# Optimization experiments

Hardware: AMD Instinct MI355X
Metric: run time of the kernel (lower is better)

Reference implementation:

```python
import jax, jax.numpy as jnp
import numpy as np

B, T, S, N, C, H = 2, 16, 256, 32, 3072, 24
D = C // H  # 128 head_dim
EPS = 1e-6


def _layernorm(x):
    # LayerNorm, elementwise_affine=False, eps=1e-6
    mu = jnp.mean(x, axis=-1, keepdims=True)
    var = jnp.mean(jnp.square(x - mu), axis=-1, keepdims=True)
    return (x - mu) * jax.lax.rsqrt(var + EPS)


def _rmsnorm(x, w):
    # RMSNorm with learnable weight, computed in fp32 (matches x.float() path)
    ms = jnp.mean(jnp.square(x), axis=-1, keepdims=True)
    return x * jax.lax.rsqrt(ms + EPS) * w


def setup_inputs() -> dict:
    key = jax.random.key(0)
    ks = jax.random.split(key, 8)
    f = lambda k, sh: jax.random.normal(k, sh, dtype=jnp.float32)
    sc = 1.0 / np.sqrt(C)
    return {
        "x": f(ks[0], (B, T * S, C)),
        "motion_vec": f(ks[1], (B, T, N, C)),
        "motion_mask": jax.random.uniform(ks[2], (B, T * S), dtype=jnp.float32),
        "w_kv": f(ks[3], (2 * C, C)) * sc,
        "b_kv": jnp.zeros((2 * C,), jnp.float32),
        "w_q": f(ks[4], (C, C)) * sc,
        "b_q": jnp.zeros((C,), jnp.float32),
        "w_o": f(ks[5], (C, C)) * sc,
        "b_o": jnp.zeros((C,), jnp.float32),
        "q_norm_w": jnp.ones((D,), jnp.float32),
        "k_norm_w": jnp.ones((D,), jnp.float32),
    }


def reference(x, motion_vec, motion_mask, w_kv, b_kv, w_q, b_q, w_o, b_o,
              q_norm_w, k_norm_w):
    x_motion = _layernorm(motion_vec)            # [B,T,N,C]
    x_feat = _layernorm(x)                       # [B,T*S,C]

    kv = x_motion @ w_kv.T + b_kv                # [B,T,N,2C]
    kv = kv.reshape(B, T, N, 2, H, D)
    k, v = kv[:, :, :, 0], kv[:, :, :, 1]        # [B,T,N,H,D]

    q = (x_feat @ w_q.T + b_q).reshape(B, T, S, H, D)
    q = _rmsnorm(q, q_norm_w)
    k = _rmsnorm(k, k_norm_w)

    # frame-local cross-attention: queries = spatial tokens, keys = motion tokens
    scale = 1.0 / jnp.sqrt(jnp.float32(D))
    scores = jnp.einsum('btshd,btnhd->bthsn', q, k) * scale  # [B,T,H,S,N]
    probs = jax.nn.softmax(scores, axis=-1)
    attn = jnp.einsum('bthsn,btnhd->btshd', probs, v)        # [B,T,S,H,D]
    attn = attn.reshape(B, T * S, C)

    out = attn @ w_o.T + b_o                     # [B,T*S,C]
    return out * motion_mask[:, :, None]
```

## Files before the change

### kernel.cpp

```cpp
#include <hip/hip_runtime.h>
#include <math.h>

typedef unsigned short u16;
typedef unsigned int u32;
typedef short bf16x8 __attribute__((ext_vector_type(8)));
typedef float f32x4 __attribute__((ext_vector_type(4)));
typedef u16 u16x4 __attribute__((ext_vector_type(4)));
typedef u16 u16x8 __attribute__((ext_vector_type(8)));
typedef u32 u32x4 __attribute__((ext_vector_type(4)));

static __device__ __forceinline__ float b2f(u16 u) {
  union { u32 i; float f; } v; v.i = ((u32)u) << 16; return v.f;
}
static __device__ __forceinline__ float blo(u32 u) {
  union { u32 i; float f; } v; v.i = u << 16; return v.f;
}
static __device__ __forceinline__ float bhi(u32 u) {
  union { u32 i; float f; } v; v.i = u & 0xffff0000u; return v.f;
}
static __device__ __forceinline__ u16 f2b(float f) {
  union { float f; u32 i; } v; v.f = f;
  u32 r = v.i + 0x7fffu + ((v.i >> 16) & 1u);
  return (u16)(r >> 16);
}

static __device__ __forceinline__ void g2l16(const void* g, void* l) {
  typedef __attribute__((address_space(1))) const void gvoid;
  typedef __attribute__((address_space(3))) void lvoid;
  __builtin_amdgcn_global_load_lds((gvoid*)g, (lvoid*)l, 16, 0, 0);
}

__global__ __launch_bounds__(256)
void wcvt_kernel(const float* __restrict__ src, u16* __restrict__ dst, int n4)
{
  for (int i = blockIdx.x * 256 + threadIdx.x; i < n4; i += gridDim.x * 256) {
    f32x4 v = *(const f32x4*)(src + (size_t)i * 4);
    u16x4 w; w.x = f2b(v.x); w.y = f2b(v.y); w.z = f2b(v.z); w.w = f2b(v.w);
    *(u16x4*)(dst + (size_t)i * 4) = w;
  }
}

__global__ __launch_bounds__(256)
void ln_kernel(const float* __restrict__ x, const float* __restrict__ mv,
               u16* __restrict__ xf, u16* __restrict__ xm)
{
  const int row = blockIdx.x, tid = threadIdx.x;
  const float* src; u16* dst;
  if (row < 8192) { src = x + (size_t)row * 3072;          dst = xf + (size_t)row * 3072; }
  else            { src = mv + (size_t)(row - 8192) * 3072; dst = xm + (size_t)(row - 8192) * 3072; }

  f32x4 vals[3];
  #pragma unroll
  for (int i = 0; i < 3; ++i) vals[i] = *(const f32x4*)(src + tid * 4 + i * 1024);

  float s1 = 0.f, s2 = 0.f;
  #pragma unroll
  for (int i = 0; i < 3; ++i) {
    f32x4 v = vals[i];
    s1 += v.x + v.y + v.z + v.w;
    s2 += v.x * v.x + v.y * v.y + v.z * v.z + v.w * v.w;
  }
  #pragma unroll
  for (int o = 32; o > 0; o >>= 1) { s1 += __shfl_down(s1, o); s2 += __shfl_down(s2, o); }
  __shared__ float r1[4], r2[4];
  const int wv = tid >> 6, ln = tid & 63;
  if (ln == 0) { r1[wv] = s1; r2[wv] = s2; }
  __syncthreads();
  const float t1 = r1[0] + r1[1] + r1[2] + r1[3];
  const float t2 = r2[0] + r2[1] + r2[2] + r2[3];
  const float mu = t1 * (1.f / 3072.f);
  const float rs = rsqrtf(t2 * (1.f / 3072.f) - mu * mu + 1e-6f);
  #pragma unroll
  for (int i = 0; i < 3; ++i) {
    f32x4 v = vals[i]; u16x4 w;
    w.x = f2b((v.x - mu) * rs); w.y = f2b((v.y - mu) * rs);
    w.z = f2b((v.z - mu) * rs); w.w = f2b((v.w - mu) * rs);
    *(u16x4*)(dst + tid * 4 + i * 1024) = w;
  }
}

template<int EPI, typename TOUT>
__global__ __launch_bounds__(256, 2)
void gemm256(const u16* __restrict__ A, const u16* __restrict__ Wb,
             const float* __restrict__ bias, const float* __restrict__ mask,
             TOUT* __restrict__ C, int M, int N, int K)
{
  __shared__ __align__(16) u16 L[36864];
  const int tid = threadIdx.x, wave = tid >> 6, lane = tid & 63;

  const int nwg = gridDim.x;
  const int bid = (blockIdx.x & 7) * (nwg >> 3) + (blockIdx.x >> 3);
  const int nbx = N >> 7;
  const int brow = (bid / nbx) << 8;
  const int bcol = (bid % nbx) << 7;
  const int wr = wave >> 1, wc = wave & 1;

  const u16* gA = A + (size_t)brow * K;
  const u16* gB = Wb + (size_t)bcol * K;

  const int srow = tid >> 2;
  const int scol = 8 * ((lane & 3) ^ ((lane >> 3) & 3));
  const int rcoff = 8 * ((lane >> 4) ^ ((lane >> 1) & 3));

  f32x4 acc[8][4] = {};

  auto STAGE = [&](int b, int tk) {
    u16* bufA = &L[b * 12288];
    u16* bufB = bufA + 8192;
    const u16* srcA = gA + tk + scol;
    const u16* srcB = gB + tk + scol;
    #pragma unroll
    for (int j = 0; j < 4; ++j)
      g2l16(srcA + (size_t)(j * 64 + srow) * K, bufA + (j * 64 + wave * 16) * 32);
    #pragma unroll
    for (int j = 0; j < 2; ++j)
      g2l16(srcB + (size_t)(j * 64 + srow) * K, bufB + (j * 64 + wave * 16) * 32);
  };

  auto COMPUTE = [&](int b) {
    const u16* bufA = &L[b * 12288];
    const u16* bufB = bufA + 8192;
    bf16x8 af[8], bfv[4];
    #pragma unroll
    for (int m = 0; m < 8; ++m)
      af[m] = *(const bf16x8*)&bufA[(wr * 128 + m * 16 + (lane & 15)) * 32 + rcoff];
    #pragma unroll
    for (int n = 0; n < 4; ++n)
      bfv[n] = *(const bf16x8*)&bufB[(wc * 64 + n * 16 + (lane & 15)) * 32 + rcoff];
    __builtin_amdgcn_s_setprio(1);
    #pragma unroll
    for (int m = 0; m < 8; ++m)
      #pragma unroll
      for (int n = 0; n < 4; ++n)
        acc[m][n] = __builtin_amdgcn_mfma_f32_16x16x32_bf16(af[m], bfv[n], acc[m][n], 0, 0, 0);
    __builtin_amdgcn_s_setprio(0);
  };

  STAGE(0, 0);
  STAGE(1, 32);
  asm volatile("s_waitcnt vmcnt(6)" ::: "memory");
  __builtin_amdgcn_s_barrier();
  __builtin_amdgcn_sched_barrier(0);

  const int NT = K >> 5;
  int cur = 0;
  for (int t = 0; t < NT; ++t) {
    const bool pf = (t + 2) < NT;
    if (pf) {
      int nb = cur + 2; if (nb >= 3) nb -= 3;
      STAGE(nb, (t + 2) << 5);
    }
    COMPUTE(cur);
    if (pf) asm volatile("s_waitcnt vmcnt(6)" ::: "memory");
    else    asm volatile("s_waitcnt vmcnt(0)" ::: "memory");
    __builtin_amdgcn_s_barrier();
    __builtin_amdgcn_sched_barrier(0);
    if (++cur == 3) cur = 0;
  }

  #pragma unroll
  for (int m = 0; m < 8; ++m) {
    const int row = brow + wr * 128 + m * 16 + ((lane >> 4) << 2);
    #pragma unroll
    for (int n = 0; n < 4; ++n) {
      const int col = bcol + wc * 64 + n * 16 + (lane & 15);
      const float bv = bias[col];
      #pragma unroll
      for (int i = 0; i < 4; ++i) {
        float v = acc[m][n][i] + bv;
        if (EPI == 1) v *= mask[row + i];
        if constexpr (__is_same(TOUT, u16))
          C[(size_t)(row + i) * N + col] = f2b(v);
        else
          C[(size_t)(row + i) * N + col] = v;
      }
    }
  }
}

template<int EPI, typename TOUT>
__global__ __launch_bounds__(256)
void gemm_mixed(const u16* __restrict__ A, const float* __restrict__ W,
                const float* __restrict__ bias, const float* __restrict__ mask,
                TOUT* __restrict__ C, int M, int N, int K)
{
  __shared__ __align__(16) u16 lA[4096];
  __shared__ __align__(16) u16 lB[4096];
  const int tid = threadIdx.x, wave = tid >> 6, lane = tid & 63;
  const int nbx = N >> 7;
  const int brow = (blockIdx.x / nbx) << 7;
  const int bcol = (blockIdx.x % nbx) << 7;
  const int wr = wave >> 1, wc = wave & 1;

  f32x4 acc[4][4] = {};
  const u16* gA = A + (size_t)brow * K;
  const float* gB = W + (size_t)bcol * K;
  const int br = tid >> 1, bk0 = (tid & 1) << 4;
  const float* bsrc0 = gB + (size_t)br * K + bk0;
  u16* bdst = &lB[br * 32 + bk0];

  for (int tk = 0; tk < K; tk += 32) {
    #pragma unroll
    for (int j = 0; j < 2; ++j) {
      const int c = j * 256 + wave * 64 + lane;
      const int r = c >> 2, k8 = (c & 3) << 3;
      g2l16(gA + (size_t)r * K + tk + k8, (char*)lA + (size_t)(j * 256 + wave * 64) * 16);
    }
    {
      const float* src = bsrc0 + tk;
      #pragma unroll
      for (int j = 0; j < 4; ++j) {
        f32x4 v = *(const f32x4*)(src + 4 * j);
        u16x4 w; w.x = f2b(v.x); w.y = f2b(v.y); w.z = f2b(v.z); w.w = f2b(v.w);
        *(u16x4*)(bdst + 4 * j) = w;
      }
    }
    __syncthreads();

    bf16x8 af[4], bfr[4];
    #pragma unroll
    for (int m = 0; m < 4; ++m)
      af[m] = *(const bf16x8*)&lA[(wr * 64 + m * 16 + (lane & 15)) * 32 + ((lane >> 4) << 3)];
    #pragma unroll
    for (int n = 0; n < 4; ++n)
      bfr[n] = *(const bf16x8*)&lB[(wc * 64 + n * 16 + (lane & 15)) * 32 + ((lane >> 4) << 3)];
    #pragma unroll
    for (int m = 0; m < 4; ++m)
      #pragma unroll
      for (int n = 0; n < 4; ++n)
        acc[m][n] = __builtin_amdgcn_mfma_f32_16x16x32_bf16(af[m], bfr[n], acc[m][n], 0, 0, 0);
    __syncthreads();
  }

  #pragma unroll
  for (int m = 0; m < 4; ++m) {
    const int row = brow + wr * 64 + m * 16 + ((lane >> 4) << 2);
    #pragma unroll
    for (int n = 0; n < 4; ++n) {
      const int col = bcol + wc * 64 + n * 16 + (lane & 15);
      const float bv = bias[col];
      #pragma unroll
      for (int i = 0; i < 4; ++i) {
        float v = acc[m][n][i] + bv;
        if (EPI == 1) v *= mask[row + i];
        if constexpr (__is_same(TOUT, u16))
          C[(size_t)(row + i) * N + col] = f2b(v);
        else
          C[(size_t)(row + i) * N + col] = v;
      }
    }
  }
}

__global__ __launch_bounds__(256)
void attn_kernel(const u16* __restrict__ qb, const u16* __restrict__ kvb,
                 const float* __restrict__ qw, const float* __restrict__ kw,
                 u16* __restrict__ attnb)
{
  __shared__ __align__(16) float Ks[32][128];
  __shared__ __align__(16) u32 Vsu[32][64];
  __shared__ float scL[256 * 33];
  const int tid = threadIdx.x;
  const int h = blockIdx.x % 24;
  const int bt = blockIdx.x / 24;

  {
    const int n = tid >> 3, sub = tid & 7;
    const size_t base = (size_t)(bt * 32 + n) * 6144 + (size_t)h * 128;
    const u16* kp = kvb + base + sub * 16;
    const u16* vp = kvb + base + 3072 + sub * 16;
    float kv_[16]; float ss = 0.f;
    u16x8 k0 = *(const u16x8*)kp;
    u16x8 k1 = *(const u16x8*)(kp + 8);
    #pragma unroll
    for (int j = 0; j < 8; ++j) { kv_[j] = b2f(k0[j]); kv_[8 + j] = b2f(k1[j]); }
    #pragma unroll
    for (int j = 0; j < 16; ++j) ss += kv_[j] * kv_[j];
    ss += __shfl_xor(ss, 1); ss += __shfl_xor(ss, 2); ss += __shfl_xor(ss, 4);
    const float krs = rsqrtf(ss * (1.f / 128.f) + 1e-6f);
    #pragma unroll
    for (int j = 0; j < 16; ++j) {
      const int d = sub * 16 + j;
      Ks[n][d] = kv_[j] * krs * kw[d] * qw[d];
    }
    u32x4 v0 = *(const u32x4*)vp;
    u32x4 v1 = *(const u32x4*)(vp + 8);
    #pragma unroll
    for (int j = 0; j < 4; ++j) { Vsu[n][sub * 8 + j] = v0[j]; Vsu[n][sub * 8 + 4 + j] = v1[j]; }
  }
  __syncthreads();

  const u16* qp = qb + (size_t)(bt * 256 + tid) * 3072 + (size_t)h * 128;
  u32 qr[64]; float qss = 0.f;
  #pragma unroll
  for (int i = 0; i < 16; ++i) {
    u32x4 t = ((const u32x4*)qp)[i];
    qr[4 * i + 0] = t.x; qr[4 * i + 1] = t.y; qr[4 * i + 2] = t.z; qr[4 * i + 3] = t.w;
  }
  #pragma unroll
  for (int i = 0; i < 64; ++i) { const float a = blo(qr[i]), b = bhi(qr[i]); qss += a * a + b * b; }
  const float qsc = rsqrtf(qss * (1.f / 128.f) + 1e-6f) * 0.08838834764831845f;

  float* mysc = &scL[tid * 33];
  for (int n2 = 0; n2 < 32; ++n2) {
    const f32x4* kr = (const f32x4*)&Ks[n2][0];
    float dot = 0.f;
    #pragma unroll
    for (int dd = 0; dd < 32; ++dd) {
      const f32x4 kk = kr[dd];
      const u32 a0 = qr[2 * dd], a1 = qr[2 * dd + 1];
      dot += blo(a0) * kk.x + bhi(a0) * kk.y + blo(a1) * kk.z + bhi(a1) * kk.w;
    }
    mysc[n2] = dot * qsc;
  }

  float p[32];
  #pragma unroll
  for (int j = 0; j < 32; ++j) p[j] = mysc[j];
  float mx = p[0];
  #pragma unroll
  for (int j = 1; j < 32; ++j) mx = fmaxf(mx, p[j]);
  float se = 0.f;
  #pragma unroll
  for (int j = 0; j < 32; ++j) { p[j] = expf(p[j] - mx); se += p[j]; }
  const float inv = 1.f / se;
  #pragma unroll
  for (int j = 0; j < 32; ++j) mysc[j] = p[j] * inv;

  u16* op = attnb + (size_t)(bt * 256 + tid) * 3072 + (size_t)h * 128;
  for (int db = 0; db < 16; ++db) {
    float o[8] = {0.f, 0.f, 0.f, 0.f, 0.f, 0.f, 0.f, 0.f};
    for (int n2 = 0; n2 < 32; ++n2) {
      const u32x4 vv = *(const u32x4*)&Vsu[n2][db * 4];
      const float pp = mysc[n2];
      o[0] += pp * blo(vv.x); o[1] += pp * bhi(vv.x);
      o[2] += pp * blo(vv.y); o[3] += pp * bhi(vv.y);
      o[4] += pp * blo(vv.z); o[5] += pp * bhi(vv.z);
      o[6] += pp * blo(vv.w); o[7] += pp * bhi(vv.w);
    }
    u16x8 w;
    #pragma unroll
    for (int j = 0; j < 8; ++j) w[j] = f2b(o[j]);
    *(u16x8*)(op + db * 8) = w;
  }
}

extern "C" void kernel_launch(void* const* d_in, const int* in_sizes, int n_in,
                              void* d_out, int out_size, void* d_ws, size_t ws_size,
                              hipStream_t stream) {
  const float* x    = (const float*)d_in[0];
  const float* mv   = (const float*)d_in[1];
  const float* mask = (const float*)d_in[2];
  const float* wkv  = (const float*)d_in[3];
  const float* bkv  = (const float*)d_in[4];
  const float* wq   = (const float*)d_in[5];
  const float* bq   = (const float*)d_in[6];
  const float* wo   = (const float*)d_in[7];
  const float* bo   = (const float*)d_in[8];
  const float* qnw  = (const float*)d_in[9];
  const float* knw  = (const float*)d_in[10];
  float* out = (float*)d_out;

  char* ws = (char*)d_ws;
  u16* xf   = (u16*)(ws);
  u16* xm   = (u16*)(ws + 50331648);
  u16* qbuf = (u16*)(ws + 56623104);
  u16* kvb  = (u16*)(ws + 106954752);
  u16* wslab = (u16*)(ws + 119537664);

  ln_kernel<<<9216, 256, 0, stream>>>(x, mv, xf, xm);

  if (ws_size >= 157286400u) {
    wcvt_kernel<<<2048, 256, 0, stream>>>(wq, wslab, 3072 * 3072 / 4);
    gemm256<0, u16><<<768, 256, 0, stream>>>(xf, wslab, bq, nullptr, qbuf, 8192, 3072, 3072);
    wcvt_kernel<<<2048, 256, 0, stream>>>(wkv, wslab, 6144 * 3072 / 4);
    gemm256<0, u16><<<192, 256, 0, stream>>>(xm, wslab, bkv, nullptr, kvb, 1024, 6144, 3072);
    attn_kernel<<<768, 256, 0, stream>>>(qbuf, kvb, qnw, knw, xf);
    wcvt_kernel<<<2048, 256, 0, stream>>>(wo, wslab, 3072 * 3072 / 4);
    gemm256<1, float><<<768, 256, 0, stream>>>(xf, wslab, bo, mask, out, 8192, 3072, 3072);
  } else {
    gemm_mixed<0, u16><<<1536, 256, 0, stream>>>(xf, wq, bq, nullptr, qbuf, 8192, 3072, 3072);
    gemm_mixed<0, u16><<<384, 256, 0, stream>>>(xm, wkv, bkv, nullptr, kvb, 1024, 6144, 3072);
    attn_kernel<<<768, 256, 0, stream>>>(qbuf, kvb, qnw, knw, xf);
    gemm_mixed<1, float><<<1536, 256, 0, stream>>>(xf, wo, bo, mask, out, 8192, 3072, 3072);
  }
}
```

Baseline: 567.4 us.

## Rewrite frame-local attention with bf16 MFMA for QK and PV

Replaces the scalar per-thread attention kernel with an MFMA-based version. Normalized K and transposed V are staged in LDS as bf16. Each wave handles 64 query rows in 16-row tiles, computing scores and P·V with 16x16x32 bf16 MFMA. Softmax uses cross-lane shuffles, and the output is staged through LDS for coalesced 16-byte stores. This removes the scalar FMA loops and the large fp32 score buffer, but adds extra bf16 rounding of the scaled Q and of the probabilities.

Measured after the change: 475.5 us. -16.2%, faster.

```diff
diff --git a/kernel.cpp b/kernel.cpp
--- a/kernel.cpp
+++ b/kernel.cpp
@@ -11,12 +11,6 @@
 
 static __device__ __forceinline__ float b2f(u16 u) {
   union { u32 i; float f; } v; v.i = ((u32)u) << 16; return v.f;
-}
-static __device__ __forceinline__ float blo(u32 u) {
-  union { u32 i; float f; } v; v.i = u << 16; return v.f;
-}
-static __device__ __forceinline__ float bhi(u32 u) {
-  union { u32 i; float f; } v; v.i = u & 0xffff0000u; return v.f;
 }
 static __device__ __forceinline__ u16 f2b(float f) {
   union { float f; u32 i; } v; v.f = f;
@@ -253,14 +247,15 @@
 }
 
 __global__ __launch_bounds__(256)
-void attn_kernel(const u16* __restrict__ qb, const u16* __restrict__ kvb,
-                 const float* __restrict__ qw, const float* __restrict__ kw,
-                 u16* __restrict__ attnb)
+void attn_mfma(const u16* __restrict__ qb, const u16* __restrict__ kvb,
+               const float* __restrict__ qw, const float* __restrict__ kw,
+               u16* __restrict__ attnb)
 {
-  __shared__ __align__(16) float Ks[32][128];
-  __shared__ __align__(16) u32 Vsu[32][64];
-  __shared__ float scL[256 * 33];
-  const int tid = threadIdx.x;
+  __shared__ __align__(16) u16 Kn[32 * 136];
+  __shared__ __align__(16) u16 Vt[128 * 40];
+  __shared__ __align__(16) u16 Pl[256 * 40];
+  __shared__ __align__(16) u16 Ol[4][16 * 136];
+  const int tid = threadIdx.x, wave = tid >> 6, lane = tid & 63;
   const int h = blockIdx.x % 24;
   const int bt = blockIdx.x / 24;
 
@@ -268,80 +263,120 @@
     const int n = tid >> 3, sub = tid & 7;
     const size_t base = (size_t)(bt * 32 + n) * 6144 + (size_t)h * 128;
     const u16* kp = kvb + base + sub * 16;
-    const u16* vp = kvb + base + 3072 + sub * 16;
-    float kv_[16]; float ss = 0.f;
     u16x8 k0 = *(const u16x8*)kp;
     u16x8 k1 = *(const u16x8*)(kp + 8);
+    float kv_[16]; float ss = 0.f;
     #pragma unroll
     for (int j = 0; j < 8; ++j) { kv_[j] = b2f(k0[j]); kv_[8 + j] = b2f(k1[j]); }
     #pragma unroll
     for (int j = 0; j < 16; ++j) ss += kv_[j] * kv_[j];
     ss += __shfl_xor(ss, 1); ss += __shfl_xor(ss, 2); ss += __shfl_xor(ss, 4);
     const float krs = rsqrtf(ss * (1.f / 128.f) + 1e-6f);
-    #pragma unroll
-    for (int j = 0; j < 16; ++j) {
+    u16x8 w0, w1;
+    #pragma unroll
+    for (int j = 0; j < 8; ++j) {
       const int d = sub * 16 + j;
-      Ks[n][d] = kv_[j] * krs * kw[d] * qw[d];
-    }
-    u32x4 v0 = *(const u32x4*)vp;
-    u32x4 v1 = *(const u32x4*)(vp + 8);
-    #pragma unroll
-    for (int j = 0; j < 4; ++j) { Vsu[n][sub * 8 + j] = v0[j]; Vsu[n][sub * 8 + 4 + j] = v1[j]; }
+      w0[j] = f2b(kv_[j] * krs * kw[d] * qw[d]);
+      w1[j] = f2b(kv_[8 + j] * krs * kw[d + 8] * qw[d + 8]);
+    }
+    *(u16x8*)&Kn[n * 136 + sub * 16] = w0;
+    *(u16x8*)&Kn[n * 136 + sub * 16 + 8] = w1;
+  }
+  {
+    const int k = tid >> 3, dc = (tid & 7) * 16;
+    const u16* vp = kvb + (size_t)(bt * 32 + k) * 6144 + (size_t)h * 128 + 3072 + dc;
+    u16x8 v0 = *(const u16x8*)vp;
+    u16x8 v1 = *(const u16x8*)(vp + 8);
+    #pragma unroll
+    for (int j = 0; j < 8; ++j) {
+      Vt[(dc + j) * 40 + k] = v0[j];
+      Vt[(dc + 8 + j) * 40 + k] = v1[j];
+    }
   }
   __syncthreads();
 
-  const u16* qp = qb + (size_t)(bt * 256 + tid) * 3072 + (size_t)h * 128;
-  u32 qr[64]; float qss = 0.f;
-  #pragma unroll
-  for (int i = 0; i < 16; ++i) {
-    u32x4 t = ((const u32x4*)qp)[i];
-    qr[4 * i + 0] = t.x; qr[4 * i + 1] = t.y; qr[4 * i + 2] = t.z; qr[4 * i + 3] = t.w;
-  }
-  #pragma unroll
-  for (int i = 0; i < 64; ++i) { const float a = blo(qr[i]), b = bhi(qr[i]); qss += a * a + b * b; }
-  const float qsc = rsqrtf(qss * (1.f / 128.f) + 1e-6f) * 0.08838834764831845f;
-
-  float* mysc = &scL[tid * 33];
-  for (int n2 = 0; n2 < 32; ++n2) {
-    const f32x4* kr = (const f32x4*)&Ks[n2][0];
-    float dot = 0.f;
-    #pragma unroll
-    for (int dd = 0; dd < 32; ++dd) {
-      const f32x4 kk = kr[dd];
-      const u32 a0 = qr[2 * dd], a1 = qr[2 * dd + 1];
-      dot += blo(a0) * kk.x + bhi(a0) * kk.y + blo(a1) * kk.z + bhi(a1) * kk.w;
-    }
-    mysc[n2] = dot * qsc;
-  }
-
-  float p[32];
-  #pragma unroll
-  for (int j = 0; j < 32; ++j) p[j] = mysc[j];
-  float mx = p[0];
-  #pragma unroll
-  for (int j = 1; j < 32; ++j) mx = fmaxf(mx, p[j]);
-  float se = 0.f;
-  #pragma unroll
-  for (int j = 0; j < 32; ++j) { p[j] = expf(p[j] - mx); se += p[j]; }
-  const float inv = 1.f / se;
-  #pragma unroll
-  for (int j = 0; j < 32; ++j) mysc[j] = p[j] * inv;
-
-  u16* op = attnb + (size_t)(bt * 256 + tid) * 3072 + (size_t)h * 128;
-  for (int db = 0; db < 16; ++db) {
-    float o[8] = {0.f, 0.f, 0.f, 0.f, 0.f, 0.f, 0.f, 0.f};
-    for (int n2 = 0; n2 < 32; ++n2) {
-      const u32x4 vv = *(const u32x4*)&Vsu[n2][db * 4];
-      const float pp = mysc[n2];
-      o[0] += pp * blo(vv.x); o[1] += pp * bhi(vv.x);
-      o[2] += pp * blo(vv.y); o[3] += pp * bhi(vv.y);
-      o[4] += pp * blo(vv.z); o[5] += pp * bhi(vv.z);
-      o[6] += pp * blo(vv.w); o[7] += pp * bhi(vv.w);
-    }
-    u16x8 w;
-    #pragma unroll
-    for (int j = 0; j < 8; ++j) w[j] = f2b(o[j]);
-    *(u16x8*)(op + db * 8) = w;
+  const int q0 = wave * 64;
+  const int lr = lane & 15, lg = lane >> 4;
+
+  for (int m = 0; m < 4; ++m) {
+    const int qrow = q0 + m * 16 + lr;
+    const u16* qp = qb + (size_t)(bt * 256 + qrow) * 3072 + (size_t)h * 128 + lg * 8;
+    bf16x8 qf[4];
+    #pragma unroll
+    for (int k = 0; k < 4; ++k) qf[k] = *(const bf16x8*)(qp + k * 32);
+    float ss = 0.f;
+    #pragma unroll
+    for (int k = 0; k < 4; ++k)
+      #pragma unroll
+      for (int j = 0; j < 8; ++j) { const float f = b2f((u16)qf[k][j]); ss += f * f; }
+    ss += __shfl_xor(ss, 16); ss += __shfl_xor(ss, 32);
+    const float qsc = rsqrtf(ss * (1.f / 128.f) + 1e-6f) * 0.08838834764831845f;
+    #pragma unroll
+    for (int k = 0; k < 4; ++k)
+      #pragma unroll
+      for (int j = 0; j < 8; ++j)
+        qf[k][j] = (short)f2b(b2f((u16)qf[k][j]) * qsc);
+
+    f32x4 s0 = {0.f, 0.f, 0.f, 0.f}, s1 = {0.f, 0.f, 0.f, 0.f};
+    #pragma unroll
+    for (int k = 0; k < 4; ++k) {
+      bf16x8 kb0 = *(const bf16x8*)&Kn[(lr) * 136 + k * 32 + lg * 8];
+      bf16x8 kb1 = *(const bf16x8*)&Kn[(16 + lr) * 136 + k * 32 + lg * 8];
+      s0 = __builtin_amdgcn_mfma_f32_16x16x32_bf16(qf[k], kb0, s0, 0, 0, 0);
+      s1 = __builtin_amdgcn_mfma_f32_16x16x32_bf16(qf[k], kb1, s1, 0, 0, 0);
+    }
+
+    float mx[4], sm[4], e0[4], e1[4];
+    #pragma unroll
+    for (int i = 0; i < 4; ++i) mx[i] = fmaxf(s0[i], s1[i]);
+    #pragma unroll
+    for (int o = 1; o <= 8; o <<= 1)
+      #pragma unroll
+      for (int i = 0; i < 4; ++i) mx[i] = fmaxf(mx[i], __shfl_xor(mx[i], o));
+    #pragma unroll
+    for (int i = 0; i < 4; ++i) {
+      e0[i] = __expf(s0[i] - mx[i]);
+      e1[i] = __expf(s1[i] - mx[i]);
+      sm[i] = e0[i] + e1[i];
+    }
+    #pragma unroll
+    for (int o = 1; o <= 8; o <<= 1)
+      #pragma unroll
+      for (int i = 0; i < 4; ++i) sm[i] += __shfl_xor(sm[i], o);
+    #pragma unroll
+    for (int i = 0; i < 4; ++i) {
+      const float inv = 1.f / sm[i];
+      const int pr = (q0 + m * 16 + lg * 4 + i) * 40;
+      Pl[pr + lr] = f2b(e0[i] * inv);
+      Pl[pr + 16 + lr] = f2b(e1[i] * inv);
+    }
+    asm volatile("s_waitcnt lgkmcnt(0)" ::: "memory");
+    __builtin_amdgcn_sched_barrier(0);
+
+    bf16x8 pf = *(const bf16x8*)&Pl[(q0 + m * 16 + lr) * 40 + lg * 8];
+    f32x4 o_[8];
+    #pragma unroll
+    for (int n = 0; n < 8; ++n) {
+      bf16x8 vb = *(const bf16x8*)&Vt[(n * 16 + lr) * 40 + lg * 8];
+      o_[n] = __builtin_amdgcn_mfma_f32_16x16x32_bf16(
+                pf, vb, (f32x4){0.f, 0.f, 0.f, 0.f}, 0, 0, 0);
+    }
+
+    u16* ow = &Ol[wave][0];
+    #pragma unroll
+    for (int n = 0; n < 8; ++n)
+      #pragma unroll
+      for (int i = 0; i < 4; ++i)
+        ow[(lg * 4 + i) * 136 + n * 16 + lr] = f2b(o_[n][i]);
+    asm volatile("s_waitcnt lgkmcnt(0)" ::: "memory");
+    __builtin_amdgcn_sched_barrier(0);
+    const int r = lane >> 2, cc = (lane & 3) * 32;
+    u16* gout = attnb + (size_t)(bt * 256 + q0 + m * 16 + r) * 3072 + (size_t)h * 128 + cc;
+    #pragma unroll
+    for (int c = 0; c < 4; ++c)
+      *(u16x8*)(gout + c * 8) = *(const u16x8*)&ow[r * 136 + cc + c * 8];
+    asm volatile("s_waitcnt lgkmcnt(0)" ::: "memory");
+    __builtin_amdgcn_sched_barrier(0);
   }
 }
 
@@ -375,13 +410,13 @@
     gemm256<0, u16><<<768, 256, 0, stream>>>(xf, wslab, bq, nullptr, qbuf, 8192, 3072, 3072);
     wcvt_kernel<<<2048, 256, 0, stream>>>(wkv, wslab, 6144 * 3072 / 4);
     gemm256<0, u16><<<192, 256, 0, stream>>>(xm, wslab, bkv, nullptr, kvb, 1024, 6144, 3072);
-    attn_kernel<<<768, 256, 0, stream>>>(qbuf, kvb, qnw, knw, xf);
+    attn_mfma<<<768, 256, 0, stream>>>(qbuf, kvb, qnw, knw, xf);
     wcvt_kernel<<<2048, 256, 0, stream>>>(wo, wslab, 3072 * 3072 / 4);
     gemm256<1, float><<<768, 256, 0, stream>>>(xf, wslab, bo, mask, out, 8192, 3072, 3072);
   } else {
     gemm_mixed<0, u16><<<1536, 256, 0, stream>>>(xf, wq, bq, nullptr, qbuf, 8192, 3072, 3072);
     gemm_mixed<0, u16><<<384, 256, 0, stream>>>(xm, wkv, bkv, nullptr, kvb, 1024, 6144, 3072);
-    attn_kernel<<<768, 256, 0, stream>>>(qbuf, kvb, qnw, knw, xf);
+    attn_mfma<<<768, 256, 0, stream>>>(qbuf, kvb, qnw, knw, xf);
     gemm_mixed<1, float><<<1536, 256, 0, stream>>>(xf, wo, bo, mask, out, 8192, 3072, 3072);
   }
 }
```
